# Optimization experiments

Hardware: AMD Instinct MI355X
Metric: run time of the kernel (lower is better)

The kernel has to match this reference:

```python
import jax, jax.numpy as jnp
import numpy as np

N_NODES = 100000


def setup_inputs() -> dict:
    key = jax.random.key(0)
    k1, k2, k3 = jax.random.split(key, 3)
    pos = jax.random.normal(k1, (N_NODES, 2), dtype=jnp.float32)
    vel = jax.random.normal(k2, (N_NODES, 2), dtype=jnp.float32)
    edge_index = jax.random.randint(k3, (2, 6400000), 0, N_NODES, dtype=jnp.int64)
    return {"pos": pos, "vel": vel, "edge_index": edge_index}


def _forward(pos, vel, edge_index):
    n = pos.shape[0]
    h = jnp.concatenate([pos, vel], axis=1)  # [N,4]
    src, dst = edge_index[0], edge_index[1]  # PyG source_to_target: h_j=src, h_i=dst
    h_i = h[dst]  # [E,4] target
    h_j = h[src]  # [E,4] source
    x0, x1 = h_i[:, 0], h_i[:, 1]
    x4, x5 = h_j[:, 0], h_j[:, 1]
    d = x4 - x0
    m0 = (d + (x1 - x5) * 0.40914905) * 0.028998906
    m1 = (d + (x1 - x5) * 0.5819344) * -0.02637788
    m2 = (x1 * -0.07907551 - d) * -0.026721993
    m3 = (x1 * 0.95594215 - x5 - x0 * 0.20244296 - x4 * -0.17809269) * 0.026933579
    msg = jnp.stack([m0, m1, m2, m3], axis=1)  # [E,4]
    # zero messages where h_i == h_j exactly (e.g. self-loops)
    same = jnp.all(h_i - h_j == 0.0, axis=1)
    msg = jnp.where(same[:, None], 0.0, msg)
    mean_in, coll = msg[:, :2], msg[:, 2:]
    add_out = jax.ops.segment_sum(coll, dst, num_segments=n)          # add-reduce ch 2,3
    sum_mean = jax.ops.segment_sum(mean_in, dst, num_segments=n)
    cnt = jax.ops.segment_sum(jnp.ones_like(dst, dtype=msg.dtype), dst, num_segments=n)
    mean_out = jnp.where(cnt[:, None] > 0, sum_mean / jnp.maximum(cnt, 1.0)[:, None], 0.0)
    aggr = jnp.concatenate([add_out, mean_out], axis=1)  # [N,4]
    # update: x0..x3 = h, x4..x7 = aggr
    y0, y1, y2, y3 = h[:, 0], h[:, 1], h[:, 2], h[:, 3]
    y4, y5, y6, y7 = aggr[:, 0], aggr[:, 1], aggr[:, 2], aggr[:, 3]
    u0 = (y1 + y7 / 0.037233025) * -0.0020586958
    u1 = ((y0 - y7 ** 2 * y5) * 0.015168043 - y6) * -0.10450508
    u2 = (y7 - y1 * 0.027931638 + y6) * 0.075265266
    u3 = (y3 ** 2 - y6 + y2 - y3 + y7 * -0.33928046) * -0.08554904
    pred0 = (u0 + u3 + u0) * -0.24326763 - u1 / 0.7301285 - u2 * 1.1234615
    pred1 = u2 - (u1 + u0) + u3
    return jnp.stack([pred0, pred1], axis=1)  # [N,2]


def reference(pos, vel, edge_index):
    return _forward(pos, vel, edge_index)
```

## Files before the change

kernel.cpp:

```cpp
#include <hip/hip_runtime.h>

typedef int int4v __attribute__((ext_vector_type(4)));
typedef unsigned long long u64;
typedef unsigned int u32;

#define FSCALE 2048.0f
#define FBIAS  8.0f
#define RBITS  8
#define RSIZE  256
#define MAXBINS 512
#define NREG   8
#define CAPX   2272
#define NSUB   4

__device__ __forceinline__ u64 pack_val(float2 ps, u32 same) {
    int fx = (int)rintf((ps.x + FBIAS) * FSCALE);
    int fy = (int)rintf((ps.y + FBIAS) * FSCALE);
    return (u64)(u32)fx | ((u64)(u32)fy << 22) | (1ULL << 44) | ((u64)same << 54);
}

__global__ __launch_bounds__(1024) void bin_edges(
    const int4v* __restrict__ src4, const int4v* __restrict__ dst4, int nvec,
    const float2* __restrict__ pos,
    u32* __restrict__ bin_ptr,
    u32* __restrict__ records,
    u64* __restrict__ acc_extra,
    int nbins)
{
    __shared__ u32 cnt[MAXBINS];
    __shared__ u32 cur[MAXBINS];
    const int reg = blockIdx.x & (NREG - 1);
    u32* my_ptr = bin_ptr + (size_t)reg * nbins;
    u32* my_rec = records + (size_t)reg * nbins * CAPX;

    int span = (nvec + gridDim.x - 1) / gridDim.x;
    int lo = blockIdx.x * span;
    int hi = lo + span; if (hi > nvec) hi = nvec;

    for (int i = threadIdx.x; i < nbins; i += 1024) cnt[i] = 0;
    __syncthreads();

    for (int i = lo + threadIdx.x; i < hi; i += 1024) {
        int4v d4 = dst4[i];
#pragma unroll
        for (int k = 0; k < 4; ++k)
            __hip_atomic_fetch_add(&cnt[((u32)d4[k]) >> RBITS], 1u,
                                   __ATOMIC_RELAXED, __HIP_MEMORY_SCOPE_WORKGROUP);
    }
    __syncthreads();

    for (int i = threadIdx.x; i < nbins; i += 1024)
        cur[i] = atomicAdd(&my_ptr[i], cnt[i]);
    __syncthreads();

    for (int i = lo + threadIdx.x; i < hi; i += 1024) {
        int4v s4 = __builtin_nontemporal_load(src4 + i);
        int4v d4 = dst4[i];
#pragma unroll
        for (int k = 0; k < 4; ++k) {
            u32 s = (u32)s4[k], d = (u32)d4[k];
            u32 bin = d >> RBITS;
            u32 slot = __hip_atomic_fetch_add(&cur[bin], 1u,
                           __ATOMIC_RELAXED, __HIP_MEMORY_SCOPE_WORKGROUP);
            if (slot < CAPX) {
                u32 rec = s | ((d & (RSIZE - 1)) << 17) | ((u32)(s == d) << 25);
                my_rec[(size_t)bin * CAPX + slot] = rec;
            } else {
                atomicAdd(acc_extra + d, pack_val(pos[s], (u32)(s == d)));
            }
        }
    }
}

__global__ __launch_bounds__(256) void reduce_bins(
    const u32* __restrict__ bin_ptr, const u32* __restrict__ records,
    const float2* __restrict__ pos, u64* __restrict__ acc, int nbins)
{
    __shared__ u64 accl[2][RSIZE];
    int bin = blockIdx.x % nbins;
    int sub = blockIdx.x / nbins;
    accl[0][threadIdx.x] = 0;
    accl[1][threadIdx.x] = 0;
    __syncthreads();
    int cp = (threadIdx.x >> 6) & 1;

#pragma unroll
    for (int rr = 0; rr < NREG / NSUB; ++rr) {
        int reg = sub + rr * NSUB;
        u32 count = bin_ptr[(size_t)reg * nbins + bin];
        if (count > CAPX) count = CAPX;
        const u32* rp = records + ((size_t)reg * nbins + bin) * CAPX;
        for (u32 r = threadIdx.x; r < count; r += 256) {
            u32 rec = rp[r];
            u32 s = rec & 0x1FFFF;
            u32 loc = (rec >> 17) & (RSIZE - 1);
            u64 val = pack_val(pos[s], rec >> 25);
            __hip_atomic_fetch_add(&accl[cp][loc], val,
                                   __ATOMIC_RELAXED, __HIP_MEMORY_SCOPE_WORKGROUP);
        }
    }
    __syncthreads();
    acc[((size_t)sub * nbins + bin) * RSIZE + threadIdx.x] =
        accl[0][threadIdx.x] + accl[1][threadIdx.x];
}

__global__ __launch_bounds__(256) void flock_edge_fb(
    const int4v* __restrict__ src4, const int4v* __restrict__ dst4, int nvec,
    const float2* __restrict__ pos, u64* __restrict__ acc)
{
    int tid = blockIdx.x * blockDim.x + threadIdx.x;
    int stride = gridDim.x * blockDim.x;
    for (int i = tid; i < nvec; i += stride) {
        int4v s4 = __builtin_nontemporal_load(src4 + i);
        int4v d4 = __builtin_nontemporal_load(dst4 + i);
#pragma unroll
        for (int k = 0; k < 4; ++k) {
            int s = s4[k], d = d4[k];
            atomicAdd(acc + d, pack_val(pos[s], (u32)(s == d)));
        }
    }
}

__global__ __launch_bounds__(256) void flock_node(
    const float2* __restrict__ pos, const float2* __restrict__ vel,
    const u64* __restrict__ acc, int nsub, int node_stride,
    const u64* __restrict__ acc_extra,
    float2* __restrict__ out, int n_nodes)
{
    int n = blockIdx.x * blockDim.x + threadIdx.x;
    if (n >= n_nodes) return;

    u64 t = acc_extra[n];
    for (int s = 0; s < nsub; ++s) t += acc[(size_t)s * node_stride + n];

    int fxi   = (int)(t & 0x3FFFFF);
    int fyi   = (int)((t >> 22) & 0x3FFFFF);
    int cnt_i = (int)((t >> 44) & 0x3FF);
    int sc_i  = (int)(t >> 54);

    float cnt = (float)cnt_i;
    float Sx  = (float)fxi * (1.0f / FSCALE) - FBIAS * cnt;
    float Sy  = (float)fyi * (1.0f / FSCALE) - FBIAS * cnt;
    float sc  = (float)sc_i;

    float2 p = pos[n];
    float2 v = vel[n];
    float x = p.x, y = p.y;

    float dsum = Sx - cnt * x;
    float esum = cnt * y - Sy;

    float sum_m0 = 0.028998906f * (dsum + esum * 0.40914905f);
    float sum_m1 = -0.02637788f * (dsum + esum * 0.5819344f);

    float sum_m3 = 0.026933579f *
        (cnt * (y * 0.95594215f - x * 0.20244296f) - Sy + 0.17809269f * Sx);
    sum_m3 -= sc * 0.026933579f *
        (y * 0.95594215f - y - x * 0.20244296f + 0.17809269f * x);

    float inv = cnt > 0.0f ? 1.0f / cnt : 0.0f;
    float y6 = sum_m0 * inv;
    float y7 = sum_m1 * inv;
    float y5 = sum_m3;

    float y0 = x, y1 = y, y2 = v.x, y3 = v.y;

    float u0 = (y1 + y7 / 0.037233025f) * -0.0020586958f;
    float u1 = ((y0 - y7 * y7 * y5) * 0.015168043f - y6) * -0.10450508f;
    float u2 = (y7 - y1 * 0.027931638f + y6) * 0.075265266f;
    float u3 = (y3 * y3 - y6 + y2 - y3 + y7 * -0.33928046f) * -0.08554904f;

    float pred0 = (u0 + u3 + u0) * -0.24326763f - u1 / 0.7301285f - u2 * 1.1234615f;
    float pred1 = u2 - (u1 + u0) + u3;

    out[n] = make_float2(pred0, pred1);
}

extern "C" void kernel_launch(void* const* d_in, const int* in_sizes, int n_in,
                              void* d_out, int out_size, void* d_ws, size_t ws_size,
                              hipStream_t stream) {
    const int n_nodes = in_sizes[0] / 2;
    const int n_edges = in_sizes[2] / 2;
    const float2* pos = (const float2*)d_in[0];
    const float2* vel = (const float2*)d_in[1];
    const int* ei = (const int*)d_in[2];
    const int* src = ei;
    const int* dst = ei + n_edges;
    const int nvec = n_edges / 4;

    const int nbins = (n_nodes + RSIZE - 1) >> RBITS;
    const int node_stride = nbins * RSIZE;

    u32* bin_ptr = (u32*)d_ws;
    u64* acc_extra = (u64*)((char*)d_ws + 16384);
    u64* acc = acc_extra + node_stride;
    u32* records = (u32*)(acc + (size_t)NSUB * node_stride);

    size_t need = 16384 + (size_t)(1 + NSUB) * node_stride * 8
                + (size_t)NREG * nbins * CAPX * 4;

    if (nbins <= MAXBINS && ws_size >= need) {
        hipMemsetAsync(d_ws, 0, 16384 + (size_t)node_stride * 8, stream);
        bin_edges<<<512, 1024, 0, stream>>>(
            (const int4v*)src, (const int4v*)dst, nvec, pos,
            bin_ptr, records, acc_extra, nbins);
        reduce_bins<<<nbins * NSUB, 256, 0, stream>>>(
            bin_ptr, records, pos, acc, nbins);
        flock_node<<<(n_nodes + 255) / 256, 256, 0, stream>>>(
            pos, vel, acc, NSUB, node_stride, acc_extra,
            (float2*)d_out, n_nodes);
    } else {
        u64* acc_fb = (u64*)d_ws;
        hipMemsetAsync(acc_fb, 0, (size_t)n_nodes * 8, stream);
        int blocks = (nvec + 255) / 256;
        if (blocks > 2048) blocks = 2048;
        flock_edge_fb<<<blocks, 256, 0, stream>>>(
            (const int4v*)src, (const int4v*)dst, nvec, pos, acc_fb);
        flock_node<<<(n_nodes + 255) / 256, 256, 0, stream>>>(
            pos, vel, acc_fb, 0, 0, acc_fb, (float2*)d_out, n_nodes);
    }
}
```

Baseline: 106.0 us.

## Replace two-pass counting binning with per-block fixed-capacity buckets of 4096 nodes

The binning kernel drops its counting pass and the global atomic offset allocation. Each of 256 blocks now writes records into its own fixed-capacity slot for each of 25 coarse buckets of 4096 destination nodes, and records per-block fill counts. The reduce kernel accumulates a whole 4096-node bucket in a 32KB shared array from 16 block-segments, then stores the partial sums in place over the records buffer, which the node kernel sums across 16 subs. This removes one full read of dst and the global atomics, but it uses more shared memory per reduce block (lower occupancy), needs more partial reads in the node kernel, and sends any overflow past the 1200-slot capacity to slow global atomics.

```diff
diff --git a/kernel.cpp b/kernel.cpp
--- a/kernel.cpp
+++ b/kernel.cpp
@@ -6,12 +6,13 @@
 
 #define FSCALE 2048.0f
 #define FBIAS  8.0f
-#define RBITS  8
-#define RSIZE  256
-#define MAXBINS 512
-#define NREG   8
-#define CAPX   2272
-#define NSUB   4
+#define BBITS  12
+#define BSIZE  4096
+#define MAXBKT 32
+#define P1B    256
+#define CAP    1200
+#define NSUB   16
+#define SEGS   (P1B / NSUB)
 
 __device__ __forceinline__ u64 pack_val(float2 ps, u32 same) {
     int fx = (int)rintf((ps.x + FBIAS) * FSCALE);
@@ -19,89 +20,74 @@
     return (u64)(u32)fx | ((u64)(u32)fy << 22) | (1ULL << 44) | ((u64)same << 54);
 }
 
-__global__ __launch_bounds__(1024) void bin_edges(
+__global__ __launch_bounds__(1024) void scatter_edges(
     const int4v* __restrict__ src4, const int4v* __restrict__ dst4, int nvec,
     const float2* __restrict__ pos,
-    u32* __restrict__ bin_ptr,
-    u32* __restrict__ records,
-    u64* __restrict__ acc_extra,
-    int nbins)
-{
-    __shared__ u32 cnt[MAXBINS];
-    __shared__ u32 cur[MAXBINS];
-    const int reg = blockIdx.x & (NREG - 1);
-    u32* my_ptr = bin_ptr + (size_t)reg * nbins;
-    u32* my_rec = records + (size_t)reg * nbins * CAPX;
+    u32* __restrict__ records, u32* __restrict__ fills ,
+    u64* __restrict__ acc_extra, int nbkt)
+{
+    __shared__ u32 cur[MAXBKT];
+    const int blk = blockIdx.x;
+    for (int i = threadIdx.x; i < nbkt; i += 1024) cur[i] = 0;
+    __syncthreads();
 
     int span = (nvec + gridDim.x - 1) / gridDim.x;
-    int lo = blockIdx.x * span;
+    int lo = blk * span;
     int hi = lo + span; if (hi > nvec) hi = nvec;
-
-    for (int i = threadIdx.x; i < nbins; i += 1024) cnt[i] = 0;
-    __syncthreads();
-
-    for (int i = lo + threadIdx.x; i < hi; i += 1024) {
-        int4v d4 = dst4[i];
-#pragma unroll
-        for (int k = 0; k < 4; ++k)
-            __hip_atomic_fetch_add(&cnt[((u32)d4[k]) >> RBITS], 1u,
-                                   __ATOMIC_RELAXED, __HIP_MEMORY_SCOPE_WORKGROUP);
-    }
-    __syncthreads();
-
-    for (int i = threadIdx.x; i < nbins; i += 1024)
-        cur[i] = atomicAdd(&my_ptr[i], cnt[i]);
-    __syncthreads();
 
     for (int i = lo + threadIdx.x; i < hi; i += 1024) {
         int4v s4 = __builtin_nontemporal_load(src4 + i);
-        int4v d4 = dst4[i];
+        int4v d4 = __builtin_nontemporal_load(dst4 + i);
 #pragma unroll
         for (int k = 0; k < 4; ++k) {
             u32 s = (u32)s4[k], d = (u32)d4[k];
-            u32 bin = d >> RBITS;
-            u32 slot = __hip_atomic_fetch_add(&cur[bin], 1u,
+            u32 b = d >> BBITS;
+            u32 slot = __hip_atomic_fetch_add(&cur[b], 1u,
                            __ATOMIC_RELAXED, __HIP_MEMORY_SCOPE_WORKGROUP);
-            if (slot < CAPX) {
-                u32 rec = s | ((d & (RSIZE - 1)) << 17) | ((u32)(s == d) << 25);
-                my_rec[(size_t)bin * CAPX + slot] = rec;
+            if (slot < CAP) {
+                u32 rec = s | ((d & (BSIZE - 1)) << 17) | ((u32)(s == d) << 29);
+                records[((size_t)b * P1B + blk) * CAP + slot] = rec;
             } else {
                 atomicAdd(acc_extra + d, pack_val(pos[s], (u32)(s == d)));
             }
         }
     }
-}
-
-__global__ __launch_bounds__(256) void reduce_bins(
-    const u32* __restrict__ bin_ptr, const u32* __restrict__ records,
-    const float2* __restrict__ pos, u64* __restrict__ acc, int nbins)
-{
-    __shared__ u64 accl[2][RSIZE];
-    int bin = blockIdx.x % nbins;
-    int sub = blockIdx.x / nbins;
-    accl[0][threadIdx.x] = 0;
-    accl[1][threadIdx.x] = 0;
-    __syncthreads();
-    int cp = (threadIdx.x >> 6) & 1;
-
-#pragma unroll
-    for (int rr = 0; rr < NREG / NSUB; ++rr) {
-        int reg = sub + rr * NSUB;
-        u32 count = bin_ptr[(size_t)reg * nbins + bin];
-        if (count > CAPX) count = CAPX;
-        const u32* rp = records + ((size_t)reg * nbins + bin) * CAPX;
+    __syncthreads();
+    for (int i = threadIdx.x; i < nbkt; i += 1024) {
+        u32 c = cur[i]; if (c > CAP) c = CAP;
+        fills[(size_t)i * P1B + blk] = c;
+    }
+}
+
+__global__ __launch_bounds__(256) void reduce_buckets(
+    u32* __restrict__ records, const u32* __restrict__ fills,
+    const float2* __restrict__ pos, int nbkt)
+{
+    __shared__ u64 accl[BSIZE];
+    int sub = blockIdx.x % NSUB;
+    int b   = blockIdx.x / NSUB;
+    for (int i = threadIdx.x; i < BSIZE; i += 256) accl[i] = 0;
+    __syncthreads();
+
+    const u32* fb = fills + (size_t)b * P1B + sub * SEGS;
+    u32* rbase = records + ((size_t)b * P1B + sub * SEGS) * CAP;
+#pragma unroll 1
+    for (int j = 0; j < SEGS; ++j) {
+        u32 count = fb[j];
+        const u32* rp = rbase + (size_t)j * CAP;
         for (u32 r = threadIdx.x; r < count; r += 256) {
             u32 rec = rp[r];
             u32 s = rec & 0x1FFFF;
-            u32 loc = (rec >> 17) & (RSIZE - 1);
-            u64 val = pack_val(pos[s], rec >> 25);
-            __hip_atomic_fetch_add(&accl[cp][loc], val,
+            u32 loc = (rec >> 17) & (BSIZE - 1);
+            u64 val = pack_val(pos[s], rec >> 29);
+            __hip_atomic_fetch_add(&accl[loc], val,
                                    __ATOMIC_RELAXED, __HIP_MEMORY_SCOPE_WORKGROUP);
         }
     }
     __syncthreads();
-    acc[((size_t)sub * nbins + bin) * RSIZE + threadIdx.x] =
-        accl[0][threadIdx.x] + accl[1][threadIdx.x];
+    u64* pdst = (u64*)rbase;
+    for (int i = threadIdx.x; i < BSIZE; i += 256)
+        pdst[i] = accl[i];
 }
 
 __global__ __launch_bounds__(256) void flock_edge_fb(
@@ -123,15 +109,18 @@
 
 __global__ __launch_bounds__(256) void flock_node(
     const float2* __restrict__ pos, const float2* __restrict__ vel,
-    const u64* __restrict__ acc, int nsub, int node_stride,
-    const u64* __restrict__ acc_extra,
-    float2* __restrict__ out, int n_nodes)
+    const u32* __restrict__ records, const u64* __restrict__ acc_extra,
+    int nsub, float2* __restrict__ out, int n_nodes)
 {
     int n = blockIdx.x * blockDim.x + threadIdx.x;
     if (n >= n_nodes) return;
 
     u64 t = acc_extra[n];
-    for (int s = 0; s < nsub; ++s) t += acc[(size_t)s * node_stride + n];
+    int b = n >> BBITS, loc = n & (BSIZE - 1);
+    for (int k = 0; k < nsub; ++k) {
+        const u64* p = (const u64*)(records + ((size_t)b * P1B + k * SEGS) * CAP);
+        t += p[loc];
+    }
 
     int fxi   = (int)(t & 0x3FFFFF);
     int fyi   = (int)((t >> 22) & 0x3FFFFF);
@@ -188,27 +177,24 @@
     const int* dst = ei + n_edges;
     const int nvec = n_edges / 4;
 
-    const int nbins = (n_nodes + RSIZE - 1) >> RBITS;
-    const int node_stride = nbins * RSIZE;
-
-    u32* bin_ptr = (u32*)d_ws;
-    u64* acc_extra = (u64*)((char*)d_ws + 16384);
-    u64* acc = acc_extra + node_stride;
-    u32* records = (u32*)(acc + (size_t)NSUB * node_stride);
-
-    size_t need = 16384 + (size_t)(1 + NSUB) * node_stride * 8
-                + (size_t)NREG * nbins * CAPX * 4;
-
-    if (nbins <= MAXBINS && ws_size >= need) {
-        hipMemsetAsync(d_ws, 0, 16384 + (size_t)node_stride * 8, stream);
-        bin_edges<<<512, 1024, 0, stream>>>(
+    const int nbkt = (n_nodes + BSIZE - 1) >> BBITS;
+    const int node_stride = nbkt * BSIZE;
+
+    u32* fills = (u32*)d_ws;
+    u64* acc_extra = (u64*)((char*)d_ws + 32768);
+    u32* records = (u32*)(acc_extra + node_stride);
+    size_t need = 32768 + (size_t)node_stride * 8
+                + (size_t)nbkt * P1B * CAP * 4;
+
+    if (nbkt <= MAXBKT && ws_size >= need) {
+        hipMemsetAsync(acc_extra, 0, (size_t)node_stride * 8, stream);
+        scatter_edges<<<P1B, 1024, 0, stream>>>(
             (const int4v*)src, (const int4v*)dst, nvec, pos,
-            bin_ptr, records, acc_extra, nbins);
-        reduce_bins<<<nbins * NSUB, 256, 0, stream>>>(
-            bin_ptr, records, pos, acc, nbins);
+            records, fills, acc_extra, nbkt);
+        reduce_buckets<<<nbkt * NSUB, 256, 0, stream>>>(
+            records, fills, pos, nbkt);
         flock_node<<<(n_nodes + 255) / 256, 256, 0, stream>>>(
-            pos, vel, acc, NSUB, node_stride, acc_extra,
-            (float2*)d_out, n_nodes);
+            pos, vel, records, acc_extra, NSUB, (float2*)d_out, n_nodes);
     } else {
         u64* acc_fb = (u64*)d_ws;
         hipMemsetAsync(acc_fb, 0, (size_t)n_nodes * 8, stream);
@@ -217,6 +203,6 @@
         flock_edge_fb<<<blocks, 256, 0, stream>>>(
             (const int4v*)src, (const int4v*)dst, nvec, pos, acc_fb);
         flock_node<<<(n_nodes + 255) / 256, 256, 0, stream>>>(
-            pos, vel, acc_fb, 0, 0, acc_fb, (float2*)d_out, n_nodes);
-    }
-}
+            pos, vel, (const u32*)d_ws, acc_fb, 0, (float2*)d_out, n_nodes);
+    }
+}
```

After: 92.12 us. 1.15x faster.
